# Kernel optimization log

Hardware: AMD Instinct MI355X
Metric: run time of the kernel (lower is better)

The kernel has to match this reference:

```python
import jax, jax.numpy as jnp
import numpy as np

L = 4        # n_layers
C = 512      # channels = d_model
NH = 16      # n_heads
DH = 32      # d_head (hard-coded in source)
DFF = 4 * C  # FeedForward hidden size
B, HH, WW = 4, 32, 32
GN_GROUPS, GN_EPS, LN_EPS = 16, 1e-6, 1e-5


def setup_inputs() -> dict:
    key = jax.random.key(0)
    ks = jax.random.split(key, 32)
    w = lambda k, s: (jax.random.normal(k, s, jnp.float32) * 0.02)
    return {
        "x": jax.random.normal(ks[0], (B, C, HH, WW), jnp.float32),
        # GroupNorm affine
        "gn_w": jnp.ones((C,), jnp.float32),
        "gn_b": jnp.zeros((C,), jnp.float32),
        # 1x1 conv in/out, stored as [C_in, C_out]
        "pin_w": w(ks[1], (C, C)), "pin_b": jnp.zeros((C,), jnp.float32),
        "pout_w": w(ks[2], (C, C)), "pout_b": jnp.zeros((C,), jnp.float32),
        # per-layer stacked params
        "ln1_w": jnp.ones((L, C), jnp.float32), "ln1_b": jnp.zeros((L, C), jnp.float32),
        "wq": w(ks[3], (L, C, C)), "wk": w(ks[4], (L, C, C)), "wv": w(ks[5], (L, C, C)),
        "wo": w(ks[6], (L, C, C)), "bo": jnp.zeros((L, C), jnp.float32),
        "ln3_w": jnp.ones((L, C), jnp.float32), "ln3_b": jnp.zeros((L, C), jnp.float32),
        "ff1_w": w(ks[7], (L, C, 2 * DFF)), "ff1_b": jnp.zeros((L, 2 * DFF), jnp.float32),
        "ff2_w": w(ks[8], (L, DFF, C)), "ff2_b": jnp.zeros((L, C), jnp.float32),
    }


def _group_norm(x, w, b):
    bsz, c, h, ww = x.shape
    xg = x.reshape(bsz, GN_GROUPS, c // GN_GROUPS, h, ww)
    m = xg.mean(axis=(2, 3, 4), keepdims=True)
    v = xg.var(axis=(2, 3, 4), keepdims=True)
    xn = ((xg - m) * jax.lax.rsqrt(v + GN_EPS)).reshape(bsz, c, h, ww)
    return xn * w[None, :, None, None] + b[None, :, None, None]


def _layer_norm(x, w, b):
    m = x.mean(axis=-1, keepdims=True)
    v = x.var(axis=-1, keepdims=True)
    return (x - m) * jax.lax.rsqrt(v + LN_EPS) * w + b


def reference(x, gn_w, gn_b, pin_w, pin_b, pout_w, pout_b,
              ln1_w, ln1_b, wq, wk, wv, wo, bo,
              ln3_w, ln3_b, ff1_w, ff1_b, ff2_w, ff2_b):
    b, c, h, w_ = x.shape
    x_in = x
    x = _group_norm(x, gn_w, gn_b)
    x = jnp.einsum('bchw,co->bohw', x, pin_w) + pin_b[None, :, None, None]
    x = x.transpose(0, 2, 3, 1).reshape(b, h * w_, c)  # [b, n, c]
    n = h * w_
    nh = c // DH
    scale = DH ** -0.5
    for l in range(L):
        hx = _layer_norm(x, ln1_w[l], ln1_b[l])
        q = (hx @ wq[l]).reshape(b, n, nh, DH)
        k = (hx @ wk[l]).reshape(b, n, nh, DH)
        v = (hx @ wv[l]).reshape(b, n, nh, DH)
        attn = jax.nn.softmax(jnp.einsum('bihd,bjhd->bhij', q, k) * scale, axis=-1)
        o = jnp.einsum('bhij,bjhd->bihd', attn, v).reshape(b, n, c)
        x = o @ wo[l] + bo[l] + x
        hx = _layer_norm(x, ln3_w[l], ln3_b[l])
        p = hx @ ff1_w[l] + ff1_b[l]
        a, g = jnp.split(p, 2, axis=-1)
        x = (a * jax.nn.gelu(g, approximate=False)) @ ff2_w[l] + ff2_b[l] + x
    x = x.reshape(b, h, w_, c).transpose(0, 3, 1, 2)
    x = jnp.einsum('bchw,co->bohw', x, pout_w) + pout_b[None, :, None, None]
    return x + x_in
```

## Files before the change

### kernel.cpp

```cpp
#include <hip/hip_runtime.h>
#include <math.h>


typedef __bf16 bf16x8_t __attribute__((ext_vector_type(8)));
typedef float f32x4 __attribute__((ext_vector_type(4)));

__device__ __forceinline__ unsigned short f2bf(float f) {
  unsigned u = __float_as_uint(f);
  return (unsigned short)((u + 0x7FFFu + ((u >> 16) & 1u)) >> 16);
}
__device__ __forceinline__ float gelu_exact(float x) {
  return 0.5f * x * (1.f + erff(x * 0.70710678118654752440f));
}

__global__ __launch_bounds__(256) void gn_stats(
    const float* __restrict__ X, const float* __restrict__ w,
    const float* __restrict__ b, float* __restrict__ sc,
    float* __restrict__ sh) {
  int blk = blockIdx.x;
  int g = blk & 15, bb = blk >> 4;
  const float4* x4 = (const float4*)(X + (size_t)blk * 32768);
  int tid = threadIdx.x;
  float sum = 0.f, sq = 0.f;
  for (int i = tid; i < 8192; i += 256) {
    float4 v = x4[i];
    sum += v.x + v.y + v.z + v.w;
    sq += v.x * v.x + v.y * v.y + v.z * v.z + v.w * v.w;
  }
  #pragma unroll
  for (int off = 32; off; off >>= 1) {
    sum += __shfl_xor(sum, off);
    sq += __shfl_xor(sq, off);
  }
  __shared__ float s0[4], s1[4];
  int wid = tid >> 6, lane = tid & 63;
  if (lane == 0) { s0[wid] = sum; s1[wid] = sq; }
  __syncthreads();
  sum = s0[0] + s0[1] + s0[2] + s0[3];
  sq = s1[0] + s1[1] + s1[2] + s1[3];
  float mean = sum * (1.f / 32768.f);
  float var = sq * (1.f / 32768.f) - mean * mean;
  float rstd = rsqrtf(var + 1e-6f);
  if (tid < 32) {
    int ch = g * 32 + tid;
    float s_ = rstd * w[ch];
    sc[bb * 512 + ch] = s_;
    sh[bb * 512 + ch] = b[ch] - mean * s_;
  }
}

struct CvtEnt {
  const float* src; unsigned short* dst;
  const float* rs; const float* rsh;
  int rows, cols, nmat, pre; float scale; size_t mstr;
};
struct CvtTab { CvtEnt e[9]; };

__global__ __launch_bounds__(256) void cvt_all(CvtTab tab) {
  __shared__ __bf16 t[32][72];
  int blk = blockIdx.x;
  int ei = 0;
  #pragma unroll
  for (int i = 1; i < 9; ++i)
    if (blk >= tab.e[i].pre) ei = i;
  const CvtEnt E = tab.e[ei];
  int local = blk - E.pre;
  int tcx = E.cols >> 5, trx = E.rows >> 6;
  int tpm = tcx * trx;
  int mat = local / tpm, tt = local - mat * tpm;
  int r0 = (tt / tcx) << 6, c0 = (tt % tcx) << 5;
  const float* sp = E.src + (size_t)mat * E.rows * E.cols;
  unsigned short* dp = E.dst + (size_t)mat * E.mstr;
  int tid = threadIdx.x;
  int r = tid >> 2, cq = (tid & 3) << 3;
  float s_ = E.scale, h_ = 0.f;
  if (E.rs) {
    s_ = E.rs[(size_t)mat * E.rows + r0 + r];
    h_ = E.rsh[(size_t)mat * E.rows + r0 + r];
  }
  const float* rowp = sp + (size_t)(r0 + r) * E.cols + c0 + cq;
  float4 a = *(const float4*)rowp;
  float4 b = *(const float4*)(rowp + 4);
  t[cq + 0][r] = (__bf16)(a.x * s_ + h_);
  t[cq + 1][r] = (__bf16)(a.y * s_ + h_);
  t[cq + 2][r] = (__bf16)(a.z * s_ + h_);
  t[cq + 3][r] = (__bf16)(a.w * s_ + h_);
  t[cq + 4][r] = (__bf16)(b.x * s_ + h_);
  t[cq + 5][r] = (__bf16)(b.y * s_ + h_);
  t[cq + 6][r] = (__bf16)(b.z * s_ + h_);
  t[cq + 7][r] = (__bf16)(b.w * s_ + h_);
  __syncthreads();
  int c = tid >> 3, r8 = (tid & 7) << 3;
  bf16x8_t v = *(const bf16x8_t*)&t[c][r8];
  *(bf16x8_t*)&dp[(size_t)(c0 + c) * E.rows + r0 + r8] = v;
}

__global__ __launch_bounds__(256) void ln_kernel(
    const float* __restrict__ X, const float* __restrict__ w,
    const float* __restrict__ b, unsigned short* __restrict__ Y) {
  int row = blockIdx.x * 4 + (threadIdx.x >> 6);
  int lane = threadIdx.x & 63;
  const float4* xr = (const float4*)(X + (size_t)row * 512);
  float4 v0 = xr[lane];
  float4 v1 = xr[lane + 64];
  float sum = v0.x + v0.y + v0.z + v0.w + v1.x + v1.y + v1.z + v1.w;
  float sq = v0.x * v0.x + v0.y * v0.y + v0.z * v0.z + v0.w * v0.w +
             v1.x * v1.x + v1.y * v1.y + v1.z * v1.z + v1.w * v1.w;
  #pragma unroll
  for (int off = 32; off; off >>= 1) {
    sum += __shfl_xor(sum, off);
    sq += __shfl_xor(sq, off);
  }
  float mean = sum * (1.f / 512.f);
  float var = sq * (1.f / 512.f) - mean * mean;
  float rstd = rsqrtf(var + 1e-5f);
  unsigned short* yr = Y + (size_t)row * 512;
  int c0 = lane * 4, c1 = lane * 4 + 256;
  const float4 w0 = *(const float4*)&w[c0], b0v = *(const float4*)&b[c0];
  const float4 w1 = *(const float4*)&w[c1], b1v = *(const float4*)&b[c1];
  unsigned p0 = (unsigned)f2bf((v0.x - mean) * rstd * w0.x + b0v.x) |
                ((unsigned)f2bf((v0.y - mean) * rstd * w0.y + b0v.y) << 16);
  unsigned p1 = (unsigned)f2bf((v0.z - mean) * rstd * w0.z + b0v.z) |
                ((unsigned)f2bf((v0.w - mean) * rstd * w0.w + b0v.w) << 16);
  unsigned p2 = (unsigned)f2bf((v1.x - mean) * rstd * w1.x + b1v.x) |
                ((unsigned)f2bf((v1.y - mean) * rstd * w1.y + b1v.y) << 16);
  unsigned p3 = (unsigned)f2bf((v1.z - mean) * rstd * w1.z + b1v.z) |
                ((unsigned)f2bf((v1.w - mean) * rstd * w1.w + b1v.w) << 16);
  uint2 q0 = {p0, p1}, q1 = {p2, p3};
  *(uint2*)&yr[c0] = q0;
  *(uint2*)&yr[c1] = q1;
}

template <int TM, int TN, int MODE>
__global__ __launch_bounds__(256) void mgemm(
    const short* __restrict__ A, int lda, const short* __restrict__ B0,
    float* C0, unsigned short* Cb, int ldc,
    const float* __restrict__ bias, const float* resid, int K, int ggoff) {
  constexpr int WM = TM / 2, WN = TN / 2, MF = WM / 16, NF = WN / 16;
  constexpr int ASL = TM / 32;
  constexpr int BSL = TN / 32;
  __shared__ short As[2][TM][64];
  __shared__ short Bs[2][TN][64];
  __shared__ short Bs2[MODE == 2 ? 2 : 1][MODE == 2 ? TN : 1][64];

  int flat = (blockIdx.z * gridDim.y + blockIdx.y) * gridDim.x + blockIdx.x;
  int xcd = flat & 7;
  int pos = flat >> 3;
  int bandH = gridDim.y >> 3;
  int m_loc = pos % bandH;
  int bn_i = pos / bandH;
  int bm = (xcd * bandH + m_loc) * TM;
  int bn = bn_i * TN;

  const short* B = B0;
  float* C = C0;
  const short* Bg = (MODE == 2) ? B0 + (size_t)ggoff * K : nullptr;
  unsigned short* Cbw = (MODE == 3) ? (unsigned short*)C : Cb;

  int tid = threadIdx.x;

  f32x4 acc[MF][NF];
  f32x4 acc2[MODE == 2 ? MF : 1][MODE == 2 ? NF : 1];
  #pragma unroll
  for (int m = 0; m < MF; ++m)
    #pragma unroll
    for (int n = 0; n < NF; ++n) {
      acc[m][n] = (f32x4)0.f;
      if (MODE == 2) acc2[m][n] = (f32x4)0.f;
    }

  int wid = tid >> 6, lane = tid & 63;
  int wr = wid >> 1, wc = wid & 1;
  int lrow = lane & 15, lhk = lane >> 4;

  bf16x8_t ra[ASL], rb[BSL], rb2[MODE == 2 ? BSL : 1];

  auto load_regs = [&](int k0) {
    #pragma unroll
    for (int i = 0; i < ASL; ++i) {
      int slot = tid + i * 256, r = slot >> 3, s = slot & 7;
      ra[i] = *(const bf16x8_t*)(A + (size_t)(bm + r) * lda + k0 + s * 8);
    }
    #pragma unroll
    for (int i = 0; i < BSL; ++i) {
      int slot = tid + i * 256, r = slot >> 3, s = slot & 7;
      rb[i] = *(const bf16x8_t*)(B + (size_t)(bn + r) * K + k0 + s * 8);
      if (MODE == 2)
        rb2[i] = *(const bf16x8_t*)(Bg + (size_t)(bn + r) * K + k0 + s * 8);
    }
  };
  auto store_lds = [&](int bufi) {
    #pragma unroll
    for (int i = 0; i < ASL; ++i) {
      int slot = tid + i * 256, r = slot >> 3, s = slot & 7;
      *(bf16x8_t*)&As[bufi][r][(s ^ (r & 7)) * 8] = ra[i];
    }
    #pragma unroll
    for (int i = 0; i < BSL; ++i) {
      int slot = tid + i * 256, r = slot >> 3, s = slot & 7;
      *(bf16x8_t*)&Bs[bufi][r][(s ^ (r & 7)) * 8] = rb[i];
      if (MODE == 2) *(bf16x8_t*)&Bs2[bufi][r][(s ^ (r & 7)) * 8] = rb2[i];
    }
  };
  auto compute = [&](int bufi) {
    bf16x8_t af[2][MF], bfr[2][NF], bf2[MODE == 2 ? 2 : 1][MODE == 2 ? NF : 1];
    #pragma unroll
    for (int ks = 0; ks < 2; ++ks) {
      int sl = ks * 4 + lhk;
      int ph = (sl ^ (lrow & 7)) * 8;
      #pragma unroll
      for (int m = 0; m < MF; ++m)
        af[ks][m] = *(const bf16x8_t*)&As[bufi][wr * WM + m * 16 + lrow][ph];
      #pragma unroll
      for (int n = 0; n < NF; ++n) {
        bfr[ks][n] = *(const bf16x8_t*)&Bs[bufi][wc * WN + n * 16 + lrow][ph];
        if (MODE == 2)
          bf2[ks][n] = *(const bf16x8_t*)&Bs2[bufi][wc * WN + n * 16 + lrow][ph];
      }
    }
    #pragma unroll
    for (int ks = 0; ks < 2; ++ks)
      #pragma unroll
      for (int m = 0; m < MF; ++m)
        #pragma unroll
        for (int n = 0; n < NF; ++n) {
          acc[m][n] = __builtin_amdgcn_mfma_f32_16x16x32_bf16(
              af[ks][m], bfr[ks][n], acc[m][n], 0, 0, 0);
          if (MODE == 2)
            acc2[m][n] = __builtin_amdgcn_mfma_f32_16x16x32_bf16(
                af[ks][m], bf2[ks][n], acc2[m][n], 0, 0, 0);
        }
  };

  int ns = K >> 6;
  load_regs(0);
  store_lds(0);
  __syncthreads();
  int buf = 0;
  for (int t = 0; t < ns; ++t) {
    bool more = (t + 1 < ns);
    if (more) load_regs((t + 1) << 6);
    compute(buf);
    if (more) store_lds(buf ^ 1);
    __syncthreads();
    buf ^= 1;
  }

  int row0 = bm + wr * WM + lhk * 4;
  int col0 = bn + wc * WN + lrow;
  unsigned short (*Lb)[TN] = (unsigned short(*)[TN])(&As[0][0][0]);
  #pragma unroll
  for (int m = 0; m < MF; ++m) {
    #pragma unroll
    for (int n = 0; n < NF; ++n) {
      int col = col0 + n * 16;
      int rl0 = wr * WM + m * 16 + lhk * 4;
      int cl = wc * WN + n * 16 + lrow;
      if (MODE == 0) {
        float bv = bias ? bias[col] : 0.f;
        #pragma unroll
        for (int j = 0; j < 4; ++j) {
          int row = row0 + m * 16 + j;
          C[(size_t)row * ldc + col] = acc[m][n][j] + bv;
        }
      } else if (MODE == 1) {
        float bv = bias[col];
        #pragma unroll
        for (int j = 0; j < 4; ++j) {
          int row = row0 + m * 16 + j;
          float v = acc[m][n][j] + bv + resid[(size_t)row * ldc + col];
          C[(size_t)row * ldc + col] = v;
          Lb[rl0 + j][cl] = f2bf(v);
        }
      } else if (MODE == 2) {
        float ba = bias[col], bg = bias[ggoff + col];
        #pragma unroll
        for (int j = 0; j < 4; ++j) {
          float a = acc[m][n][j] + ba;
          float g = acc2[m][n][j] + bg;
          Lb[rl0 + j][cl] = f2bf(a * gelu_exact(g));
        }
      } else if (MODE == 3) {
        #pragma unroll
        for (int j = 0; j < 4; ++j) Lb[rl0 + j][cl] = f2bf(acc[m][n][j]);
      } else if (MODE == 4) {
        float bv = bias[col];
        int row = row0 + m * 16;
        int b_ = row >> 10, n0 = row & 1023;
        size_t oidx = ((size_t)b_ * 512 + col) * 1024 + n0;
        float4 xi = *(const float4*)&resid[oidx];
        float4 ov = {acc[m][n][0] + bv + xi.x, acc[m][n][1] + bv + xi.y,
                     acc[m][n][2] + bv + xi.z, acc[m][n][3] + bv + xi.w};
        *(float4*)&C[oidx] = ov;
      } else {
        float bv = bias[col];
        #pragma unroll
        for (int j = 0; j < 4; ++j) {
          int row = row0 + m * 16 + j;
          C[(size_t)row * ldc + col] =
              acc[m][n][j] + bv + resid[(size_t)row * ldc + col];
        }
      }
    }
  }
  if (MODE == 1 || MODE == 2 || MODE == 3) {
    __syncthreads();
    constexpr int CQ = TN / 8;
    #pragma unroll
    for (int i = 0; i < TM * TN / 8 / 256; ++i) {
      int slot = tid + i * 256;
      int r = slot / CQ, cq = (slot % CQ) * 8;
      *(bf16x8_t*)&Cbw[(size_t)(bm + r) * ldc + bn + cq] =
          *(const bf16x8_t*)&Lb[r][cq];
    }
  }
}

__global__ __launch_bounds__(256) void fattn_kernel(
    const unsigned short* __restrict__ QKV, unsigned short* __restrict__ O) {
  constexpr int KT = 64, LDQ = 1536;
  __shared__ __bf16 Ks[2][KT][40];
  __shared__ __bf16 Vs[2][32][68];
  __shared__ __bf16 Ps[4][16][68];

  int h = blockIdx.y, bb = blockIdx.z;
  int q0 = blockIdx.x * 64;
  int tid = threadIdx.x;
  int wid = tid >> 6, lane = tid & 63;
  int lrow = lane & 15, lhk = lane >> 4;

  const unsigned short* Qb = QKV + (size_t)bb * 1024 * LDQ + h * 32;
  const unsigned short* Kb = Qb + 512;
  const unsigned short* Vb = Qb + 1024;

  bf16x8_t qa = *(const bf16x8_t*)(
      Qb + (size_t)(q0 + wid * 16 + lrow) * LDQ + lhk * 8);

  int kr = tid >> 2, kp = tid & 3;
  int vk = tid & 63, vd0 = (tid >> 6) * 8;

  bf16x8_t kreg, vreg;
  auto gload = [&](int kt) {
    kreg = *(const bf16x8_t*)(Kb + (size_t)(kt + kr) * LDQ + kp * 8);
    vreg = *(const bf16x8_t*)(Vb + (size_t)(kt + vk) * LDQ + vd0);
  };
  auto sstore = [&](int bufi) {
    *(bf16x8_t*)&Ks[bufi][kr][kp * 8] = kreg;
    #pragma unroll
    for (int i = 0; i < 8; ++i) Vs[bufi][vd0 + i][vk] = vreg[i];
  };

  f32x4 o[2];
  float lpart[4];
  o[0] = (f32x4)0.f;
  o[1] = (f32x4)0.f;
  #pragma unroll
  for (int j = 0; j < 4; ++j) lpart[j] = 0.f;

  gload(0);
  sstore(0);
  __syncthreads();
  for (int t = 0; t < 16; ++t) {
    int buf = t & 1;
    if (t < 15) gload((t + 1) * KT);

    bf16x8_t kb[4];
    #pragma unroll
    for (int n = 0; n < 4; ++n)
      kb[n] = *(const bf16x8_t*)&Ks[buf][n * 16 + lrow][lhk * 8];
    f32x4 s[4];
    __builtin_amdgcn_s_setprio(1);
    #pragma unroll
    for (int n = 0; n < 4; ++n)
      s[n] = __builtin_amdgcn_mfma_f32_16x16x32_bf16(qa, kb[n], (f32x4)0.f, 0,
                                                     0, 0);
    __builtin_amdgcn_s_setprio(0);

    #pragma unroll
    for (int j = 0; j < 4; ++j) {
      float p0 = exp2f(s[0][j]), p1 = exp2f(s[1][j]);
      float p2 = exp2f(s[2][j]), p3 = exp2f(s[3][j]);
      lpart[j] += (p0 + p1) + (p2 + p3);
      int prow = lhk * 4 + j;
      Ps[wid][prow][lrow] = (__bf16)p0;
      Ps[wid][prow][16 + lrow] = (__bf16)p1;
      Ps[wid][prow][32 + lrow] = (__bf16)p2;
      Ps[wid][prow][48 + lrow] = (__bf16)p3;
    }

    __builtin_amdgcn_s_setprio(1);
    #pragma unroll
    for (int ks = 0; ks < 2; ++ks) {
      bf16x8_t pa = *(const bf16x8_t*)&Ps[wid][lrow][ks * 32 + lhk * 8];
      #pragma unroll
      for (int dn = 0; dn < 2; ++dn) {
        bf16x8_t vbf =
            *(const bf16x8_t*)&Vs[buf][dn * 16 + lrow][ks * 32 + lhk * 8];
        o[dn] =
            __builtin_amdgcn_mfma_f32_16x16x32_bf16(pa, vbf, o[dn], 0, 0, 0);
      }
    }
    __builtin_amdgcn_s_setprio(0);

    if (t < 15) sstore(buf ^ 1);
    __syncthreads();
  }

  #pragma unroll
  for (int j = 0; j < 4; ++j) {
    float l = lpart[j];
    #pragma unroll
    for (int off = 1; off < 16; off <<= 1) l += __shfl_xor(l, off);
    float inv = 1.f / l;
    int row = q0 + wid * 16 + lhk * 4 + j;
    #pragma unroll
    for (int dn = 0; dn < 2; ++dn)
      O[(size_t)(bb * 1024 + row) * 512 + h * 32 + dn * 16 + lrow] =
          __builtin_bit_cast(unsigned short, (__bf16)(o[dn][j] * inv));
  }
}

extern "C" void kernel_launch(void* const* d_in, const int* in_sizes, int n_in,
                              void* d_out, int out_size, void* d_ws,
                              size_t ws_size, hipStream_t stream) {
  const float* x_in = (const float*)d_in[0];
  const float* gn_w = (const float*)d_in[1];
  const float* gn_b = (const float*)d_in[2];
  const float* pin_w = (const float*)d_in[3];
  const float* pin_b = (const float*)d_in[4];
  const float* pout_w = (const float*)d_in[5];
  const float* pout_b = (const float*)d_in[6];
  const float* ln1_w = (const float*)d_in[7];
  const float* ln1_b = (const float*)d_in[8];
  const float* wq = (const float*)d_in[9];
  const float* wk = (const float*)d_in[10];
  const float* wv = (const float*)d_in[11];
  const float* wo = (const float*)d_in[12];
  const float* bo = (const float*)d_in[13];
  const float* ln3_w = (const float*)d_in[14];
  const float* ln3_b = (const float*)d_in[15];
  const float* ff1_w = (const float*)d_in[16];
  const float* ff1_b = (const float*)d_in[17];
  const float* ff2_w = (const float*)d_in[18];
  const float* ff2_b = (const float*)d_in[19];

  char* wsb = (char*)d_ws;
  float* XTOK = (float*)wsb;
  char* R = wsb + (8u << 20);
  unsigned short* QKVb = (unsigned short*)R;
  unsigned short* G2b = (unsigned short*)R;
  float* gnsc = (float*)(R + (16u << 20));
  float* gnsh = gnsc + 2048;
  unsigned short* XTb = (unsigned short*)(wsb + (32u << 20));
  unsigned short* HXb = (unsigned short*)(wsb + (36u << 20));
  unsigned short* Obf = (unsigned short*)(wsb + (40u << 20));
  unsigned short* XTOKb = (unsigned short*)(wsb + (44u << 20));
  unsigned short* W = (unsigned short*)(wsb + (48u << 20));
  const size_t S = 262144;
  unsigned short* pinT = W;
  unsigned short* poutT = W + S;
  unsigned short* wqkvT = W + 2 * S;
  unsigned short* woT = wqkvT + 12 * S;
  unsigned short* ff1T = woT + 4 * S;
  unsigned short* ff2T = ff1T + 32 * S;

  const float qscale = 0.17677669529663687f * 1.4426950408889634f;

  gn_stats<<<64, 256, 0, stream>>>(x_in, gn_w, gn_b, gnsc, gnsh);

  CvtTab tab;
  int pre = 0;
  auto add = [&](int i, const float* src, unsigned short* dst, int rows,
                 int cols, int nmat, float sc, const float* rs,
                 const float* rsh, size_t mstr) {
    tab.e[i] = {src, dst, rs, rsh, rows, cols, nmat, pre, sc, mstr};
    pre += nmat * (rows / 64) * (cols / 32);
  };
  add(0, x_in, XTb, 512, 1024, 4, 1.f, gnsc, gnsh, 512 * 1024);
  add(1, pin_w, pinT, 512, 512, 1, 1.f, nullptr, nullptr, S);
  add(2, pout_w, poutT, 512, 512, 1, 1.f, nullptr, nullptr, S);
  add(3, wq, wqkvT, 512, 512, 4, qscale, nullptr, nullptr, 3 * S);
  add(4, wk, wqkvT + S, 512, 512, 4, 1.f, nullptr, nullptr, 3 * S);
  add(5, wv, wqkvT + 2 * S, 512, 512, 4, 1.f, nullptr, nullptr, 3 * S);
  add(6, wo, woT, 512, 512, 4, 1.f, nullptr, nullptr, S);
  add(7, ff1_w, ff1T, 512, 4096, 4, 1.f, nullptr, nullptr, 8 * S);
  add(8, ff2_w, ff2T, 2048, 512, 4, 1.f, nullptr, nullptr, 4 * S);
  cvt_all<<<pre, 256, 0, stream>>>(tab);

  mgemm<128, 64, 0><<<dim3(8, 32, 1), 256, 0, stream>>>(
      (const short*)XTb, 512, (const short*)pinT, XTOK, nullptr, 512, pin_b,
      nullptr, 512, 0);

  for (int l = 0; l < 4; ++l) {
    const short* wqkvT_l = (const short*)(wqkvT + (size_t)l * 3 * S);
    const short* woT_l = (const short*)(woT + (size_t)l * S);
    const short* ff1T_l = (const short*)(ff1T + (size_t)l * 8 * S);
    const short* ff2T_l = (const short*)(ff2T + (size_t)l * 4 * S);

    ln_kernel<<<1024, 256, 0, stream>>>(XTOK, ln1_w + l * 512, ln1_b + l * 512,
                                        HXb);
    mgemm<128, 128, 3><<<dim3(12, 32, 1), 256, 0, stream>>>(
        (const short*)HXb, 512, wqkvT_l, (float*)QKVb, nullptr, 1536, nullptr,
        nullptr, 512, 0);
    fattn_kernel<<<dim3(16, 16, 4), 256, 0, stream>>>(QKVb, Obf);
    mgemm<128, 64, 5><<<dim3(8, 32, 1), 256, 0, stream>>>(
        (const short*)Obf, 512, woT_l, XTOK, nullptr, 512, bo + l * 512, XTOK,
        512, 0);
    ln_kernel<<<1024, 256, 0, stream>>>(XTOK, ln3_w + l * 512, ln3_b + l * 512,
                                        HXb);
    mgemm<128, 64, 2><<<dim3(32, 32, 1), 256, 0, stream>>>(
        (const short*)HXb, 512, ff1T_l, nullptr, G2b, 2048, ff1_b + l * 4096,
        nullptr, 512, 2048);
    if (l < 3) {
      mgemm<128, 64, 5><<<dim3(8, 32, 1), 256, 0, stream>>>(
          (const short*)G2b, 2048, ff2T_l, XTOK, nullptr, 512, ff2_b + l * 512,
          XTOK, 2048, 0);
    } else {
      mgemm<128, 64, 1><<<dim3(8, 32, 1), 256, 0, stream>>>(
          (const short*)G2b, 2048, ff2T_l, XTOK, XTOKb, 512, ff2_b + l * 512,
          XTOK, 2048, 0);
    }
  }
  mgemm<128, 64, 4><<<dim3(8, 32, 1), 256, 0, stream>>>(
      (const short*)XTOKb, 512, (const short*)poutT, (float*)d_out, nullptr,
      512, pout_b, x_in, 512, 0);
}
```

Measured before the change: 547.4 us.

## Switch GEMM kernel to 32x32x16 MFMA tiles and pad LDS rows

```diff
diff --git a/kernel.cpp b/kernel.cpp
--- a/kernel.cpp
+++ b/kernel.cpp
@@ -4,6 +4,7 @@
 
 typedef __bf16 bf16x8_t __attribute__((ext_vector_type(8)));
 typedef float f32x4 __attribute__((ext_vector_type(4)));
+typedef float f32x16 __attribute__((ext_vector_type(16)));
 
 __device__ __forceinline__ unsigned short f2bf(float f) {
   unsigned u = __float_as_uint(f);
@@ -136,12 +137,13 @@
     const short* __restrict__ A, int lda, const short* __restrict__ B0,
     float* C0, unsigned short* Cb, int ldc,
     const float* __restrict__ bias, const float* resid, int K, int ggoff) {
-  constexpr int WM = TM / 2, WN = TN / 2, MF = WM / 16, NF = WN / 16;
+  constexpr int WM = TM / 2, WN = TN / 2, MF = WM / 32, NF = WN / 32;
   constexpr int ASL = TM / 32;
   constexpr int BSL = TN / 32;
-  __shared__ short As[2][TM][64];
-  __shared__ short Bs[2][TN][64];
-  __shared__ short Bs2[MODE == 2 ? 2 : 1][MODE == 2 ? TN : 1][64];
+  constexpr int LP = 68;
+  __shared__ short As[2][TM][LP];
+  __shared__ short Bs[2][TN][LP];
+  __shared__ short Bs2[MODE == 2 ? 2 : 1][MODE == 2 ? TN : 1][LP];
 
   int flat = (blockIdx.z * gridDim.y + blockIdx.y) * gridDim.x + blockIdx.x;
   int xcd = flat & 7;
@@ -159,19 +161,19 @@
 
   int tid = threadIdx.x;
 
-  f32x4 acc[MF][NF];
-  f32x4 acc2[MODE == 2 ? MF : 1][MODE == 2 ? NF : 1];
+  f32x16 acc[MF][NF];
+  f32x16 acc2[MODE == 2 ? MF : 1][MODE == 2 ? NF : 1];
   #pragma unroll
   for (int m = 0; m < MF; ++m)
     #pragma unroll
     for (int n = 0; n < NF; ++n) {
-      acc[m][n] = (f32x4)0.f;
-      if (MODE == 2) acc2[m][n] = (f32x4)0.f;
+      acc[m][n] = (f32x16)0.f;
+      if (MODE == 2) acc2[m][n] = (f32x16)0.f;
     }
 
   int wid = tid >> 6, lane = tid & 63;
   int wr = wid >> 1, wc = wid & 1;
-  int lrow = lane & 15, lhk = lane >> 4;
+  int l31 = lane & 31, l2 = lane >> 5;
 
   bf16x8_t ra[ASL], rb[BSL], rb2[MODE == 2 ? BSL : 1];
 
@@ -203,33 +205,33 @@
     }
   };
   auto compute = [&](int bufi) {
-    bf16x8_t af[2][MF], bfr[2][NF], bf2[MODE == 2 ? 2 : 1][MODE == 2 ? NF : 1];
-    #pragma unroll
-    for (int ks = 0; ks < 2; ++ks) {
-      int sl = ks * 4 + lhk;
-      int ph = (sl ^ (lrow & 7)) * 8;
+    #pragma unroll
+    for (int ks = 0; ks < 4; ++ks) {
+      int sl = ks * 2 + l2;
+      bf16x8_t af[MF], bfr[NF], bf2v[MODE == 2 ? NF : 1];
       #pragma unroll
-      for (int m = 0; m < MF; ++m)
-        af[ks][m] = *(const bf16x8_t*)&As[bufi][wr * WM + m * 16 + lrow][ph];
+      for (int m = 0; m < MF; ++m) {
+        int r = wr * WM + m * 32 + l31;
+        af[m] = *(const bf16x8_t*)&As[bufi][r][(sl ^ (r & 7)) * 8];
+      }
       #pragma unroll
       for (int n = 0; n < NF; ++n) {
-        bfr[ks][n] = *(const bf16x8_t*)&Bs[bufi][wc * WN + n * 16 + lrow][ph];
+        int r = wc * WN + n * 32 + l31;
+        bfr[n] = *(const bf16x8_t*)&Bs[bufi][r][(sl ^ (r & 7)) * 8];
         if (MODE == 2)
-          bf2[ks][n] = *(const bf16x8_t*)&Bs2[bufi][wc * WN + n * 16 + lrow][ph];
+          bf2v[n] = *(const bf16x8_t*)&Bs2[bufi][r][(sl ^ (r & 7)) * 8];
       }
-    }
-    #pragma unroll
-    for (int ks = 0; ks < 2; ++ks)
       #pragma unroll
       for (int m = 0; m < MF; ++m)
         #pragma unroll
         for (int n = 0; n < NF; ++n) {
-          acc[m][n] = __builtin_amdgcn_mfma_f32_16x16x32_bf16(
-              af[ks][m], bfr[ks][n], acc[m][n], 0, 0, 0);
+          acc[m][n] = __builtin_amdgcn_mfma_f32_32x32x16_bf16(
+              af[m], bfr[n], acc[m][n], 0, 0, 0);
           if (MODE == 2)
-            acc2[m][n] = __builtin_amdgcn_mfma_f32_16x16x32_bf16(
-                af[ks][m], bf2[ks][n], acc2[m][n], 0, 0, 0);
+            acc2[m][n] = __builtin_amdgcn_mfma_f32_32x32x16_bf16(
+                af[m], bf2v[n], acc2[m][n], 0, 0, 0);
         }
+    }
   };
 
   int ns = K >> 6;
@@ -246,59 +248,63 @@
     buf ^= 1;
   }
 
-  int row0 = bm + wr * WM + lhk * 4;
-  int col0 = bn + wc * WN + lrow;
   unsigned short (*Lb)[TN] = (unsigned short(*)[TN])(&As[0][0][0]);
   #pragma unroll
   for (int m = 0; m < MF; ++m) {
     #pragma unroll
     for (int n = 0; n < NF; ++n) {
-      int col = col0 + n * 16;
-      int rl0 = wr * WM + m * 16 + lhk * 4;
-      int cl = wc * WN + n * 16 + lrow;
-      if (MODE == 0) {
-        float bv = bias ? bias[col] : 0.f;
-        #pragma unroll
-        for (int j = 0; j < 4; ++j) {
-          int row = row0 + m * 16 + j;
-          C[(size_t)row * ldc + col] = acc[m][n][j] + bv;
-        }
-      } else if (MODE == 1) {
-        float bv = bias[col];
-        #pragma unroll
-        for (int j = 0; j < 4; ++j) {
-          int row = row0 + m * 16 + j;
-          float v = acc[m][n][j] + bv + resid[(size_t)row * ldc + col];
-          C[(size_t)row * ldc + col] = v;
-          Lb[rl0 + j][cl] = f2bf(v);
-        }
-      } else if (MODE == 2) {
-        float ba = bias[col], bg = bias[ggoff + col];
-        #pragma unroll
-        for (int j = 0; j < 4; ++j) {
-          float a = acc[m][n][j] + ba;
-          float g = acc2[m][n][j] + bg;
-          Lb[rl0 + j][cl] = f2bf(a * gelu_exact(g));
-        }
-      } else if (MODE == 3) {
-        #pragma unroll
-        for (int j = 0; j < 4; ++j) Lb[rl0 + j][cl] = f2bf(acc[m][n][j]);
-      } else if (MODE == 4) {
-        float bv = bias[col];
-        int row = row0 + m * 16;
-        int b_ = row >> 10, n0 = row & 1023;
-        size_t oidx = ((size_t)b_ * 512 + col) * 1024 + n0;
-        float4 xi = *(const float4*)&resid[oidx];
-        float4 ov = {acc[m][n][0] + bv + xi.x, acc[m][n][1] + bv + xi.y,
-                     acc[m][n][2] + bv + xi.z, acc[m][n][3] + bv + xi.w};
-        *(float4*)&C[oidx] = ov;
-      } else {
-        float bv = bias[col];
-        #pragma unroll
-        for (int j = 0; j < 4; ++j) {
-          int row = row0 + m * 16 + j;
-          C[(size_t)row * ldc + col] =
-              acc[m][n][j] + bv + resid[(size_t)row * ldc + col];
+      int cl = wc * WN + n * 32 + l31;
+      int col = bn + cl;
+      #pragma unroll
+      for (int g = 0; g < 4; ++g) {
+        int rl0 = wr * WM + m * 32 + l2 * 4 + g * 8;
+        if (MODE == 0) {
+          float bv = bias ? bias[col] : 0.f;
+          #pragma unroll
+          for (int q = 0; q < 4; ++q) {
+            int row = bm + rl0 + q;
+            C[(size_t)row * ldc + col] = acc[m][n][g * 4 + q] + bv;
+          }
+        } else if (MODE == 1) {
+          float bv = bias[col];
+          #pragma unroll
+          for (int q = 0; q < 4; ++q) {
+            int row = bm + rl0 + q;
+            float v = acc[m][n][g * 4 + q] + bv + resid[(size_t)row * ldc + col];
+            C[(size_t)row * ldc + col] = v;
+            Lb[rl0 + q][cl] = f2bf(v);
+          }
+        } else if (MODE == 2) {
+          float ba = bias[col], bg = bias[ggoff + col];
+          #pragma unroll
+          for (int q = 0; q < 4; ++q) {
+            float a = acc[m][n][g * 4 + q] + ba;
+            float gg = acc2[m][n][g * 4 + q] + bg;
+            Lb[rl0 + q][cl] = f2bf(a * gelu_exact(gg));
+          }
+        } else if (MODE == 3) {
+          #pragma unroll
+          for (int q = 0; q < 4; ++q)
+            Lb[rl0 + q][cl] = f2bf(acc[m][n][g * 4 + q]);
+        } else if (MODE == 4) {
+          float bv = bias[col];
+          int row = bm + rl0;
+          int b_ = row >> 10, n0 = row & 1023;
+          size_t oidx = ((size_t)b_ * 512 + col) * 1024 + n0;
+          float4 xi = *(const float4*)&resid[oidx];
+          float4 ov = {acc[m][n][g * 4 + 0] + bv + xi.x,
+                       acc[m][n][g * 4 + 1] + bv + xi.y,
+                       acc[m][n][g * 4 + 2] + bv + xi.z,
+                       acc[m][n][g * 4 + 3] + bv + xi.w};
+          *(float4*)&C[oidx] = ov;
+        } else {
+          float bv = bias[col];
+          #pragma unroll
+          for (int q = 0; q < 4; ++q) {
+            int row = bm + rl0 + q;
+            C[(size_t)row * ldc + col] =
+                acc[m][n][g * 4 + q] + bv + resid[(size_t)row * ldc + col];
+          }
         }
       }
     }
```

After: 579.6 us. 1.06x slower.
